# Kernel tuning notes

Measured on AMD Instinct MI355X. Metric: run time of the kernel, lower is better.

Reference implementation:

```python
import jax, jax.numpy as jnp
import numpy as np


def setup_inputs() -> dict:
    key = jax.random.key(0)
    k1, k2, k3 = jax.random.split(key, 3)
    B, IN, OUT = 8192, 2048, 2048
    x = jax.random.normal(k1, (B, IN), dtype=jnp.float32)
    # kaiming_uniform_(a=sqrt(5)) on [OUT, IN] -> bound = sqrt(6/((1+5)*IN)) = 1/sqrt(IN)
    wb = 1.0 / np.sqrt(IN)
    weight = jax.random.uniform(k2, (OUT, IN), dtype=jnp.float32, minval=-wb, maxval=wb)
    bb = 1.0 / np.sqrt(IN)
    bias = jax.random.uniform(k3, (OUT,), dtype=jnp.float32, minval=-bb, maxval=bb)
    return {"x": x, "weight": weight, "bias": bias}


def reference(x, weight, bias):
    # out[b,o] = sum_i (x[b,i] + w[o,i]) = rowsum(x)[b] + rowsum(w)[o]
    # (identical math to the O(B*O*I) broadcast-sum, computed in O(B*I + O*I + B*O))
    x_sum = jnp.sum(x, axis=1)        # [B]
    w_sum = jnp.sum(weight, axis=1)   # [O]
    out = x_sum[:, None] + w_sum[None, :]  # [B, O]
    out = out * bias                  # note: original does `output *= self.bias`
    return out
```

## Files before the change

### kernel.cpp

```cpp
#include <hip/hip_runtime.h>


#define B_DIM 8192
#define IN_DIM 2048
#define OUT_DIM 2048
#define ROWS_PER_WAVE 4

typedef float f32x4 __attribute__((ext_vector_type(4)));

__device__ __forceinline__ float butterfly_reduce(float s) {
    #pragma unroll
    for (int off = 32; off; off >>= 1)
        s += __shfl_xor(s, off, 64);
    return s;
}

__device__ __forceinline__ void load_row(f32x4 (&v)[8], const float* __restrict__ row,
                                         int lane) {
    const f32x4* r4 = reinterpret_cast<const f32x4*>(row);
    #pragma unroll
    for (int k = 0; k < 8; ++k)
        v[k] = r4[lane + (k << 6)];
}

__device__ __forceinline__ float reduce_row(const f32x4 (&v)[8]) {
    float s = 0.f;
    #pragma unroll
    for (int k = 0; k < 8; ++k)
        s += (v[k].x + v[k].y) + (v[k].z + v[k].w);
    return butterfly_reduce(s);
}

__global__ __launch_bounds__(256) void wsb_kernel(const float* __restrict__ w,
                                                  const float* __restrict__ bias,
                                                  float* __restrict__ wsb) {
    const int wave = threadIdx.x >> 6;
    const int lane = threadIdx.x & 63;
    const int row  = (blockIdx.x << 2) + wave;
    f32x4 v[8];
    load_row(v, w + (size_t)row * IN_DIM, lane);
    float s = reduce_row(v);
    if (lane == 0)
        wsb[row] = s * bias[row];
}

__global__ __launch_bounds__(256) void fused_row_kernel(const float* __restrict__ x,
                                                        const float* __restrict__ bias,
                                                        const float* __restrict__ wsb,
                                                        f32x4* __restrict__ out4) {
    const int wave = threadIdx.x >> 6;
    const int lane = threadIdx.x & 63;
    const int row0 = ((blockIdx.x << 2) + wave) * ROWS_PER_WAVE;
    const f32x4* bias4 = reinterpret_cast<const f32x4*>(bias);
    const f32x4* wsb4  = reinterpret_cast<const f32x4*>(wsb);

    f32x4 cur[8], nxt[8];
    load_row(cur, x + (size_t)row0 * IN_DIM, lane);

    #pragma unroll
    for (int r = 0; r < ROWS_PER_WAVE; ++r) {
        if (r + 1 < ROWS_PER_WAVE)
            load_row(nxt, x + (size_t)(row0 + r + 1) * IN_DIM, lane);

        const float xs = reduce_row(cur);

        f32x4* orow = out4 + (size_t)(row0 + r) * (OUT_DIM / 4);
        #pragma unroll
        for (int k = 0; k < 8; ++k) {
            const int i = lane + (k << 6);
            const f32x4 bi = bias4[i];
            const f32x4 wv = wsb4[i];
            f32x4 o;
            o.x = fmaf(xs, bi.x, wv.x);
            o.y = fmaf(xs, bi.y, wv.y);
            o.z = fmaf(xs, bi.z, wv.z);
            o.w = fmaf(xs, bi.w, wv.w);
            orow[i] = o;
        }

        #pragma unroll
        for (int k = 0; k < 8; ++k)
            cur[k] = nxt[k];
    }
}

extern "C" void kernel_launch(void* const* d_in, const int* in_sizes, int n_in,
                              void* d_out, int out_size, void* d_ws, size_t ws_size,
                              hipStream_t stream) {
    const float* x    = (const float*)d_in[0];
    const float* w    = (const float*)d_in[1];
    const float* bias = (const float*)d_in[2];
    float* out = (float*)d_out;
    float* wsb = (float*)d_ws;

    wsb_kernel<<<OUT_DIM / 4, 256, 0, stream>>>(w, bias, wsb);
    fused_row_kernel<<<B_DIM / (4 * ROWS_PER_WAVE), 256, 0, stream>>>(x, bias, wsb,
                                                                     (f32x4*)out);
}
```

Baseline: 30.51 us.

## Split x and weight row-sums into one kernel, then a pure broadcast-write kernel

Moves the x row reductions out of the output-writing kernel into a combined row-sum kernel that reduces both x and weight rows, one wave per row. A separate write kernel then reads the x sums and writes the output with each thread holding its bias and wsb values in registers. The aim is to expose more parallelism for the 64MB x read and to make the 64MB output write a simple streaming pass. The cost is an extra round trip of the x sums through global memory and the loss of overlap between reading x and writing the output within one kernel.

```diff
diff --git a/kernel.cpp b/kernel.cpp
--- a/kernel.cpp
+++ b/kernel.cpp
@@ -4,7 +4,6 @@
 #define B_DIM 8192
 #define IN_DIM 2048
 #define OUT_DIM 2048
-#define ROWS_PER_WAVE 4
 
 typedef float f32x4 __attribute__((ext_vector_type(4)));
 
@@ -15,15 +14,12 @@
     return s;
 }
 
-__device__ __forceinline__ void load_row(f32x4 (&v)[8], const float* __restrict__ row,
-                                         int lane) {
+__device__ __forceinline__ float row_reduce(const float* __restrict__ row, int lane) {
     const f32x4* r4 = reinterpret_cast<const f32x4*>(row);
+    f32x4 v[8];
     #pragma unroll
     for (int k = 0; k < 8; ++k)
         v[k] = r4[lane + (k << 6)];
-}
-
-__device__ __forceinline__ float reduce_row(const f32x4 (&v)[8]) {
     float s = 0.f;
     #pragma unroll
     for (int k = 0; k < 8; ++k)
@@ -31,56 +27,54 @@
     return butterfly_reduce(s);
 }
 
-__global__ __launch_bounds__(256) void wsb_kernel(const float* __restrict__ w,
-                                                  const float* __restrict__ bias,
-                                                  float* __restrict__ wsb) {
-    const int wave = threadIdx.x >> 6;
+__global__ __launch_bounds__(256) void rowsum_kernel(const float* __restrict__ x,
+                                                     const float* __restrict__ w,
+                                                     const float* __restrict__ bias,
+                                                     float* __restrict__ xsum,
+                                                     float* __restrict__ wsb) {
+    const int wid  = (blockIdx.x << 2) + (threadIdx.x >> 6);
     const int lane = threadIdx.x & 63;
-    const int row  = (blockIdx.x << 2) + wave;
-    f32x4 v[8];
-    load_row(v, w + (size_t)row * IN_DIM, lane);
-    float s = reduce_row(v);
-    if (lane == 0)
-        wsb[row] = s * bias[row];
+    if (wid < B_DIM) {
+        float s = row_reduce(x + (size_t)wid * IN_DIM, lane);
+        if (lane == 0) xsum[wid] = s;
+    } else {
+        const int o = wid - B_DIM;
+        float s = row_reduce(w + (size_t)o * IN_DIM, lane);
+        if (lane == 0) wsb[o] = s * bias[o];
+    }
 }
 
-__global__ __launch_bounds__(256) void fused_row_kernel(const float* __restrict__ x,
-                                                        const float* __restrict__ bias,
-                                                        const float* __restrict__ wsb,
-                                                        f32x4* __restrict__ out4) {
-    const int wave = threadIdx.x >> 6;
-    const int lane = threadIdx.x & 63;
-    const int row0 = ((blockIdx.x << 2) + wave) * ROWS_PER_WAVE;
+__global__ __launch_bounds__(256) void write_kernel(const float* __restrict__ xsum,
+                                                    const float* __restrict__ bias,
+                                                    const float* __restrict__ wsb,
+                                                    f32x4* __restrict__ out4) {
+    const int tid  = threadIdx.x;
+    const int rbase = blockIdx.x << 2;
     const f32x4* bias4 = reinterpret_cast<const f32x4*>(bias);
     const f32x4* wsb4  = reinterpret_cast<const f32x4*>(wsb);
 
-    f32x4 cur[8], nxt[8];
-    load_row(cur, x + (size_t)row0 * IN_DIM, lane);
+    const f32x4 b0 = bias4[tid];
+    const f32x4 b1 = bias4[tid + 256];
+    const f32x4 w0 = wsb4[tid];
+    const f32x4 w1 = wsb4[tid + 256];
+
+    const f32x4 xs4 = *reinterpret_cast<const f32x4*>(&xsum[rbase]);
 
     #pragma unroll
-    for (int r = 0; r < ROWS_PER_WAVE; ++r) {
-        if (r + 1 < ROWS_PER_WAVE)
-            load_row(nxt, x + (size_t)(row0 + r + 1) * IN_DIM, lane);
-
-        const float xs = reduce_row(cur);
-
-        f32x4* orow = out4 + (size_t)(row0 + r) * (OUT_DIM / 4);
-        #pragma unroll
-        for (int k = 0; k < 8; ++k) {
-            const int i = lane + (k << 6);
-            const f32x4 bi = bias4[i];
-            const f32x4 wv = wsb4[i];
-            f32x4 o;
-            o.x = fmaf(xs, bi.x, wv.x);
-            o.y = fmaf(xs, bi.y, wv.y);
-            o.z = fmaf(xs, bi.z, wv.z);
-            o.w = fmaf(xs, bi.w, wv.w);
-            orow[i] = o;
-        }
-
-        #pragma unroll
-        for (int k = 0; k < 8; ++k)
-            cur[k] = nxt[k];
+    for (int r = 0; r < 4; ++r) {
+        const float xs = xs4[r];
+        f32x4* orow = out4 + (size_t)(rbase + r) * (OUT_DIM / 4);
+        f32x4 o0, o1;
+        o0.x = fmaf(xs, b0.x, w0.x);
+        o0.y = fmaf(xs, b0.y, w0.y);
+        o0.z = fmaf(xs, b0.z, w0.z);
+        o0.w = fmaf(xs, b0.w, w0.w);
+        o1.x = fmaf(xs, b1.x, w1.x);
+        o1.y = fmaf(xs, b1.y, w1.y);
+        o1.z = fmaf(xs, b1.z, w1.z);
+        o1.w = fmaf(xs, b1.w, w1.w);
+        orow[tid]       = o0;
+        orow[tid + 256] = o1;
     }
 }
 
@@ -90,10 +84,10 @@
     const float* x    = (const float*)d_in[0];
     const float* w    = (const float*)d_in[1];
     const float* bias = (const float*)d_in[2];
-    float* out = (float*)d_out;
-    float* wsb = (float*)d_ws;
+    float* out  = (float*)d_out;
+    float* xsum = (float*)d_ws;
+    float* wsb  = xsum + B_DIM;
 
-    wsb_kernel<<<OUT_DIM / 4, 256, 0, stream>>>(w, bias, wsb);
-    fused_row_kernel<<<B_DIM / (4 * ROWS_PER_WAVE), 256, 0, stream>>>(x, bias, wsb,
-                                                                     (f32x4*)out);
+    rowsum_kernel<<<(B_DIM + OUT_DIM) / 4, 256, 0, stream>>>(x, w, bias, xsum, wsb);
+    write_kernel<<<B_DIM / 4, 256, 0, stream>>>(xsum, bias, wsb, (f32x4*)out);
 }
```

After: 29.62 us. -2.9%, faster.
